# Performance work log

Hardware: AMD Instinct MI355X
Metric: run time of the kernel (lower is better)

The kernel has to match this reference:

```python
import jax, jax.numpy as jnp
import numpy as np

B, T, IN_DIM = 128, 512, 32
H = 256            # h_dim; bidirectional -> embedding_dim D = 2*H = 512
N_EMB = 1024
BETA = 0.25


def setup_inputs() -> dict:
    key = jax.random.key(0)
    ks = jax.random.split(key, 12)
    traj = jax.random.normal(ks[0], (B, T, IN_DIM), dtype=jnp.float32)
    # variable-length padding mask: ones up to length, zeros after
    lengths = jax.random.randint(ks[1], (B,), 1, T + 1)
    mask = (jnp.arange(T)[None, :] < lengths[:, None]).astype(jnp.int32)
    s_x = 1.0 / np.sqrt(H)
    def u(k, shape):
        return jax.random.uniform(k, shape, jnp.float32, -s_x, s_x)
    # PyTorch GRU param layout: W_ih [3H, in], W_hh [3H, H], biases [3H]
    Wx_f, Wh_f = u(ks[2], (3 * H, IN_DIM)), u(ks[3], (3 * H, H))
    bx_f, bh_f = u(ks[4], (3 * H,)), u(ks[5], (3 * H,))
    Wx_b, Wh_b = u(ks[6], (3 * H, IN_DIM)), u(ks[7], (3 * H, H))
    bx_b, bh_b = u(ks[8], (3 * H,)), u(ks[9], (3 * H,))
    # codebook: nn.Embedding(n_embeddings, D) with uniform(-1/n, 1/n) init
    codebook = jax.random.uniform(ks[10], (N_EMB, 2 * H), jnp.float32,
                                  -1.0 / N_EMB, 1.0 / N_EMB)
    return {"traj": traj, "mask": mask,
            "Wx_f": Wx_f, "Wh_f": Wh_f, "bx_f": bx_f, "bh_f": bh_f,
            "Wx_b": Wx_b, "Wh_b": Wh_b, "bx_b": bx_b, "bh_b": bh_b,
            "codebook": codebook}


def _gru_dir(x, Wx, Wh, bx, bh):
    """Single-direction GRU over time (PyTorch gate math). x: [B,T,in] -> [B,T,H]."""
    b, t, _ = x.shape
    h_dim = Wh.shape[1]
    xg = jnp.einsum('bti,gi->btg', x, Wx) + bx  # precompute input gates [B,T,3H]
    def step(h, xg_t):
        hg = h @ Wh.T + bh
        xr, xz, xn = jnp.split(xg_t, 3, axis=-1)
        hr, hz, hn = jnp.split(hg, 3, axis=-1)
        r = jax.nn.sigmoid(xr + hr)
        z = jax.nn.sigmoid(xz + hz)
        n = jnp.tanh(xn + r * hn)
        h_new = (1.0 - z) * n + z * h
        return h_new, h_new
    h0 = jnp.zeros((b, h_dim), x.dtype)
    _, hs = jax.lax.scan(step, h0, jnp.swapaxes(xg, 0, 1))  # [T,B,H]
    return jnp.swapaxes(hs, 0, 1)


def _encode(traj, Wx_f, Wh_f, bx_f, bh_f, Wx_b, Wh_b, bx_b, bh_b):
    out_f = _gru_dir(traj, Wx_f, Wh_f, bx_f, bh_f)
    out_b = jnp.flip(_gru_dir(jnp.flip(traj, axis=1), Wx_b, Wh_b, bx_b, bh_b), axis=1)
    return jnp.concatenate([out_f, out_b], axis=-1)  # [B,T,2H]


def _vq(z_e, codebook, beta):
    # d(z, e) = |z|^2 + |e|^2 - 2 z.e  -> argmin over codebook
    d = (jnp.sum(z_e ** 2, axis=1, keepdims=True)
         + jnp.sum(codebook ** 2, axis=1)[None, :]
         - 2.0 * z_e @ codebook.T)                      # [B, N_EMB]
    idx = jnp.argmin(d, axis=1)                         # [B]
    z_q = codebook[idx]                                 # gather [B, D]
    loss = (jnp.mean((jax.lax.stop_gradient(z_q) - z_e) ** 2)
            + beta * jnp.mean((z_q - jax.lax.stop_gradient(z_e)) ** 2))
    z_q_st = z_e + jax.lax.stop_gradient(z_q - z_e)     # straight-through
    counts = jnp.zeros((codebook.shape[0],), z_e.dtype).at[idx].add(1.0)
    p = counts / z_e.shape[0]
    perplexity = jnp.exp(-jnp.sum(p * jnp.log(p + 1e-10)))
    return loss, z_q_st, perplexity, idx


def reference(traj, mask, Wx_f, Wh_f, bx_f, bh_f, Wx_b, Wh_b, bx_b, bh_b, codebook):
    z_e = _encode(traj, Wx_f, Wh_f, bx_f, bh_f, Wx_b, Wh_b, bx_b, bh_b)  # [B,T,2H]
    t = mask.shape[1]
    # last index where mask == 1:  T-1 - argmax(flip(mask))
    last_real_index = t - 1 - jnp.argmax(jnp.flip(mask, axis=1), axis=1)
    z_e_last = z_e[jnp.arange(z_e.shape[0]), last_real_index]            # [B,2H]
    loss, z_q, perplexity, _ = _vq(z_e_last, codebook, BETA)
    return z_q, loss, perplexity
```

## Files before the change

kernel.cpp:

```cpp
#include <hip/hip_runtime.h>
#include <math.h>

constexpr int B  = 128;
constexpr int T  = 512;
constexpr int IN = 32;
constexpr int H  = 256;
constexpr int D  = 2 * H;
constexpr int NC = 1024;

constexpr int NG   = 64;
constexpr int GW   = 4;
constexpr int SEQ  = 4;
constexpr int NTHR = 768;

constexpr int LDS_PAD_BYTES = 28672;


__global__ void k_zero(int* __restrict__ counts, double* __restrict__ lsum,
                       unsigned long long* __restrict__ slab) {
    const int i = blockIdx.x * 256 + threadIdx.x;
    if (i < NC) counts[i] = 0;
    if (i == 0) *lsum = 0.0;
    slab[i] = 0ull;
}

__global__ void k_lengths(const int* __restrict__ mask, int* __restrict__ last) {
    const int b = blockIdx.x;
    const int t = threadIdx.x;
    int s = 0;
    #pragma unroll
    for (int m = 0; m < T / 64; ++m) s += mask[b * T + m * 64 + t];
    #pragma unroll
    for (int off = 32; off > 0; off >>= 1) s += __shfl_down(s, off, 64);
    if (t == 0) last[b] = s - 1;
}

__global__ void k_plan(const int* __restrict__ last, int* __restrict__ plan,
                       int* __restrict__ slen, int* __restrict__ glen) {
    __shared__ int ll[B];
    const int t = threadIdx.x;
    ll[t] = last[t];
    __syncthreads();
    const int lf = ll[t] + 1;
    const int lb = T - ll[t];
    int rf = 0, rb = 0;
    for (int j = 0; j < B; ++j) {
        const int ljf = ll[j] + 1, ljb = T - ll[j];
        rf += (ljf > lf) || (ljf == lf && j < t);
        rb += (ljb > lb) || (ljb == lb && j < t);
    }
    plan[rf] = t;       slen[rf] = lf;
    plan[128 + rb] = t; slen[128 + rb] = lb;
    if ((rf & 3) == 0) glen[rf >> 2] = lf;
    if ((rb & 3) == 0) glen[32 + (rb >> 2)] = lb;
}

__global__ void k_transpose(float* __restrict__ dst, const float* __restrict__ src,
                            int rows, int cols) {
    const int idx = blockIdx.x * 256 + threadIdx.x;
    const int r = idx % rows;
    const int c = idx / rows;
    dst[idx] = src[r * cols + c];
}

__global__ void k_cbn2(const float* __restrict__ cb, double* __restrict__ cbn2) {
    const int c = blockIdx.x * 256 + threadIdx.x;
    double s = 0.0;
    for (int k = 0; k < D; ++k) {
        const double e = (double)cb[c * D + k];
        s += e * e;
    }
    cbn2[c] = s;
}


__device__ __forceinline__ float sigmoidf_(float x) {
    return 1.0f / (1.0f + expf(-x));
}

__global__ __launch_bounds__(NTHR, 3) void k_gru(
    const float* __restrict__ traj,
    const float* __restrict__ Whf, const float* __restrict__ Whb,
    const float* __restrict__ Wxf, const float* __restrict__ Wxb,
    const float* __restrict__ bxf, const float* __restrict__ bhf,
    const float* __restrict__ bxb, const float* __restrict__ bhb,
    const int* __restrict__ plan, const int* __restrict__ slen,
    const int* __restrict__ glen,
    unsigned long long* __restrict__ hgt,
    float* __restrict__ ze)
{
    extern __shared__ float dynpad[];
    (void)dynpad;

    const int g   = blockIdx.x & 63;
    const int w   = blockIdx.x >> 6;
    const int dir = (g >= 32) ? 1 : 0;

    const float* __restrict__ Wh = dir ? Whb : Whf;
    const float* __restrict__ Wx = dir ? Wxb : Wxf;
    const float* __restrict__ bx = dir ? bxb : bxf;
    const float* __restrict__ bh = dir ? bhb : bhf;

    const int tid = threadIdx.x;
    const int kq  = tid / 96;
    const int rp  = tid - kq * 96;
    const int lr0 = 2 * rp;
    const int gi  = lr0 >> 6;
    const int Rg0 = gi * H + w * 64 + (lr0 & 63);

    __shared__ float4 h4[SEQ][64];
    __shared__ float  P [8][SEQ][194];
    __shared__ float  Px[8][SEQ][194];
    __shared__ float4 xb4[2][SEQ][8];
    __shared__ int    bbS[SEQ], lsS[SEQ];

    if (tid < SEQ) { bbS[tid] = plan[g * 4 + tid]; lsS[tid] = slen[g * 4 + tid]; }
    {
        float2* hp = (float2*)h4;
        if (tid < 512) hp[tid] = make_float2(0.0f, 0.0f);
    }
    const int L = glen[g];

    float4 wh[16];
    {
        const float4* p0 = (const float4*)(Wh + (size_t)Rg0 * 256 + kq * 32);
        const float4* p1 = (const float4*)(Wh + (size_t)(Rg0 + 1) * 256 + kq * 32);
        #pragma unroll
        for (int i = 0; i < 8; ++i) { wh[i] = p0[i]; wh[8 + i] = p1[i]; }
    }
    const float4 wx0 = *(const float4*)(Wx + Rg0 * 32 + kq * 4);
    const float4 wx1 = *(const float4*)(Wx + (Rg0 + 1) * 32 + kq * 4);

    float bxr = 0, bxz = 0, bxn = 0, bhr = 0, bhz = 0, bhn = 0;
    if (tid < 256) {
        const int j2 = tid & 63;
        bxr = bx[w * 64 + j2]; bxz = bx[H + w * 64 + j2]; bxn = bx[2 * H + w * 64 + j2];
        bhr = bh[w * 64 + j2]; bhz = bh[H + w * 64 + j2]; bhn = bh[2 * H + w * 64 + j2];
    }
    __syncthreads();
    if (tid < 128) {
        const int s = tid >> 5, i = tid & 31;
        const int t0 = dir ? (T - 1) : 0;
        ((float*)xb4)[128 + s * 32 + i] = traj[(bbS[s] * T + t0) * IN + i];
    }
    __syncthreads();

    const int u = tid - 256;

    for (int step = 1; step <= L; ++step) {
        const int buf = step & 1;
        unsigned long long* __restrict__ slab =
            hgt + (buf * NG + g) * (GW * SEQ * 64);

        float4 a0 = {0,0,0,0}, a1 = {0,0,0,0}, a2 = {0,0,0,0}, a3 = {0,0,0,0};
        float4 c0 = {0,0,0,0}, c1 = {0,0,0,0}, c2 = {0,0,0,0}, c3 = {0,0,0,0};
        #pragma unroll
        for (int i = 0; i < 8; ++i) {
            const float4 w0 = wh[i];
            const float4 w1 = wh[8 + i];
            float4 hv;
            hv = h4[0][kq * 8 + i];
            a0.x = fmaf(w0.x, hv.x, a0.x); a0.y = fmaf(w0.y, hv.y, a0.y);
            a0.z = fmaf(w0.z, hv.z, a0.z); a0.w = fmaf(w0.w, hv.w, a0.w);
            c0.x = fmaf(w1.x, hv.x, c0.x); c0.y = fmaf(w1.y, hv.y, c0.y);
            c0.z = fmaf(w1.z, hv.z, c0.z); c0.w = fmaf(w1.w, hv.w, c0.w);
            hv = h4[1][kq * 8 + i];
            a1.x = fmaf(w0.x, hv.x, a1.x); a1.y = fmaf(w0.y, hv.y, a1.y);
            a1.z = fmaf(w0.z, hv.z, a1.z); a1.w = fmaf(w0.w, hv.w, a1.w);
            c1.x = fmaf(w1.x, hv.x, c1.x); c1.y = fmaf(w1.y, hv.y, c1.y);
            c1.z = fmaf(w1.z, hv.z, c1.z); c1.w = fmaf(w1.w, hv.w, c1.w);
            hv = h4[2][kq * 8 + i];
            a2.x = fmaf(w0.x, hv.x, a2.x); a2.y = fmaf(w0.y, hv.y, a2.y);
            a2.z = fmaf(w0.z, hv.z, a2.z); a2.w = fmaf(w0.w, hv.w, a2.w);
            c2.x = fmaf(w1.x, hv.x, c2.x); c2.y = fmaf(w1.y, hv.y, c2.y);
            c2.z = fmaf(w1.z, hv.z, c2.z); c2.w = fmaf(w1.w, hv.w, c2.w);
            hv = h4[3][kq * 8 + i];
            a3.x = fmaf(w0.x, hv.x, a3.x); a3.y = fmaf(w0.y, hv.y, a3.y);
            a3.z = fmaf(w0.z, hv.z, a3.z); a3.w = fmaf(w0.w, hv.w, a3.w);
            c3.x = fmaf(w1.x, hv.x, c3.x); c3.y = fmaf(w1.y, hv.y, c3.y);
            c3.z = fmaf(w1.z, hv.z, c3.z); c3.w = fmaf(w1.w, hv.w, c3.w);
        }
        {
            float4 xv;
            float2 pv;
            xv = xb4[buf][0][kq];
            pv.x = a0.x + a0.y + a0.z + a0.w;
            pv.y = c0.x + c0.y + c0.z + c0.w;
            *(float2*)&P[kq][0][lr0] = pv;
            pv.x = wx0.x * xv.x + wx0.y * xv.y + wx0.z * xv.z + wx0.w * xv.w;
            pv.y = wx1.x * xv.x + wx1.y * xv.y + wx1.z * xv.z + wx1.w * xv.w;
            *(float2*)&Px[kq][0][lr0] = pv;
            xv = xb4[buf][1][kq];
            pv.x = a1.x + a1.y + a1.z + a1.w;
            pv.y = c1.x + c1.y + c1.z + c1.w;
            *(float2*)&P[kq][1][lr0] = pv;
            pv.x = wx0.x * xv.x + wx0.y * xv.y + wx0.z * xv.z + wx0.w * xv.w;
            pv.y = wx1.x * xv.x + wx1.y * xv.y + wx1.z * xv.z + wx1.w * xv.w;
            *(float2*)&Px[kq][1][lr0] = pv;
            xv = xb4[buf][2][kq];
            pv.x = a2.x + a2.y + a2.z + a2.w;
            pv.y = c2.x + c2.y + c2.z + c2.w;
            *(float2*)&P[kq][2][lr0] = pv;
            pv.x = wx0.x * xv.x + wx0.y * xv.y + wx0.z * xv.z + wx0.w * xv.w;
            pv.y = wx1.x * xv.x + wx1.y * xv.y + wx1.z * xv.z + wx1.w * xv.w;
            *(float2*)&Px[kq][2][lr0] = pv;
            xv = xb4[buf][3][kq];
            pv.x = a3.x + a3.y + a3.z + a3.w;
            pv.y = c3.x + c3.y + c3.z + c3.w;
            *(float2*)&P[kq][3][lr0] = pv;
            pv.x = wx0.x * xv.x + wx0.y * xv.y + wx0.z * xv.z + wx0.w * xv.w;
            pv.y = wx1.x * xv.x + wx1.y * xv.y + wx1.z * xv.z + wx1.w * xv.w;
            *(float2*)&Px[kq][3][lr0] = pv;
        }
        __syncthreads();

        if (tid < 256) {
            const int j2 = tid & 63, s = tid >> 6;
            float hr = 0.f, hz = 0.f, hn_ = 0.f, xr = 0.f, xz = 0.f, xn = 0.f;
            #pragma unroll
            for (int kk = 0; kk < 8; ++kk) {
                hr  += P [kk][s][j2];
                hz  += P [kk][s][64 + j2];
                hn_ += P [kk][s][128 + j2];
                xr  += Px[kk][s][j2];
                xz  += Px[kk][s][64 + j2];
                xn  += Px[kk][s][128 + j2];
            }
            const float r = sigmoidf_(xr + bxr + hr + bhr);
            const float z = sigmoidf_(xz + bxz + hz + bhz);
            const float n = tanhf(xn + bxn + r * (hn_ + bhn));
            const int jg = w * 64 + j2;
            const float hp = ((const float*)h4)[s * 256 + jg];
            const float hnew = (1.0f - z) * n + z * hp;
            ((float*)h4)[s * 256 + jg] = hnew;
            union { float f; unsigned ui; } cv; cv.f = hnew;
            const unsigned long long pk =
                ((unsigned long long)(unsigned)step << 32) | cv.ui;
            __hip_atomic_store(&slab[w * 256 + s * 64 + j2], pk,
                               __ATOMIC_RELAXED, __HIP_MEMORY_SCOPE_AGENT);
            if (step == lsS[s]) ze[bbS[s] * D + dir * H + jg] = hnew;
        } else {
            float xval = 0.0f;
            int xs = 0, xi = 0;
            const bool do_x = (u < 128) && (step < L);
            if (do_x) {
                xs = u >> 5; xi = u & 31;
                const int tn = dir ? (T - 1 - step) : step;
                xval = traj[(bbS[xs] * T + tn) * IN + xi];
            }
            const int p0 = u >> 8;
            const int r2 = u & 255;
            const int s0 = r2 >> 6, j0 = r2 & 63;
            const int pw0 = p0 + (p0 >= w ? 1 : 0);
            unsigned long long* ad0 = &slab[pw0 * 256 + s0 * 64 + j0];
            if (u < 256) {
                const int pw1 = 2 + (2 >= w ? 1 : 0);
                unsigned long long* ad1 = &slab[pw1 * 256 + s0 * 64 + j0];
                unsigned long long v0 = 0, v1 = 0;
                bool d0 = false, d1 = false;
                do {
                    if (!d0) { v0 = __hip_atomic_load(ad0, __ATOMIC_RELAXED,
                                   __HIP_MEMORY_SCOPE_AGENT); d0 = ((int)(v0 >> 32) >= step); }
                    if (!d1) { v1 = __hip_atomic_load(ad1, __ATOMIC_RELAXED,
                                   __HIP_MEMORY_SCOPE_AGENT); d1 = ((int)(v1 >> 32) >= step); }
                } while (!(d0 && d1));
                union { unsigned ui; float f; } e0, e1;
                e0.ui = (unsigned)v0; e1.ui = (unsigned)v1;
                ((float*)h4)[s0 * 256 + pw0 * 64 + j0] = e0.f;
                ((float*)h4)[s0 * 256 + pw1 * 64 + j0] = e1.f;
            } else {
                unsigned long long v0;
                do {
                    v0 = __hip_atomic_load(ad0, __ATOMIC_RELAXED,
                                           __HIP_MEMORY_SCOPE_AGENT);
                } while ((int)(v0 >> 32) < step);
                union { unsigned ui; float f; } e0; e0.ui = (unsigned)v0;
                ((float*)h4)[s0 * 256 + pw0 * 64 + j0] = e0.f;
            }
            if (do_x)
                ((float*)xb4)[(buf ^ 1) * 128 + xs * 32 + xi] = xval;
        }
        __syncthreads();
    }
}


__global__ __launch_bounds__(256) void k_vq(
    const float* __restrict__ ze, const float* __restrict__ cbT,
    const float* __restrict__ cb, const double* __restrict__ cbn2,
    int* __restrict__ counts, double* __restrict__ lsum,
    float* __restrict__ out)
{
    __shared__ float lz[D];
    __shared__ double ds[256];
    __shared__ int cs[256];

    const int b = blockIdx.x;
    const int t = threadIdx.x;

    lz[t]       = ze[b * D + t];
    lz[t + 256] = ze[b * D + 256 + t];
    __syncthreads();

    double best = 1e300;
    int bc = 0;
    for (int m = 0; m < NC / 256; ++m) {
        const int c = m * 256 + t;
        double s2 = 0.0;
        #pragma unroll 4
        for (int k = 0; k < D; ++k)
            s2 += (double)lz[k] * (double)cbT[k * NC + c];
        const double dist = cbn2[c] - 2.0 * s2;
        if (dist < best) { best = dist; bc = c; }
    }
    ds[t] = best; cs[t] = bc;
    __syncthreads();
    for (int s = 128; s > 0; s >>= 1) {
        if (t < s) {
            if (ds[t + s] < ds[t] || (ds[t + s] == ds[t] && cs[t + s] < cs[t])) {
                ds[t] = ds[t + s]; cs[t] = cs[t + s];
            }
        }
        __syncthreads();
    }
    const int idx = cs[0];
    __syncthreads();

    if (t == 0) atomicAdd(&counts[idx], 1);

    double loc = 0.0;
    for (int jj = t; jj < D; jj += 256) {
        const float zev = lz[jj];
        const float zqv = cb[idx * D + jj];
        out[b * D + jj] = zev + (zqv - zev);
        const double df = (double)zqv - (double)zev;
        loc += df * df;
    }
    ds[t] = loc;
    __syncthreads();
    for (int s = 128; s > 0; s >>= 1) {
        if (t < s) ds[t] += ds[t + s];
        __syncthreads();
    }
    if (t == 0) atomicAdd(lsum, ds[0]);
}

__global__ void k_final(const int* __restrict__ counts,
                        const double* __restrict__ lsum,
                        float* __restrict__ out)
{
    __shared__ double ds[256];
    const int t = threadIdx.x;
    double s = 0.0;
    for (int c = t; c < NC; c += 256) {
        const double p = (double)counts[c] / (double)B;
        s += p * log(p + 1e-10);
    }
    ds[t] = s;
    __syncthreads();
    for (int r = 128; r > 0; r >>= 1) {
        if (t < r) ds[t] += ds[t + r];
        __syncthreads();
    }
    if (t == 0) {
        out[B * D]     = (float)(lsum[0] * 1.25 / (double)(B * D));
        out[B * D + 1] = (float)exp(-ds[0]);
    }
}


extern "C" void kernel_launch(void* const* d_in, const int* in_sizes, int n_in,
                              void* d_out, int out_size, void* d_ws, size_t ws_size,
                              hipStream_t stream) {
    const float* traj = (const float*)d_in[0];
    const int*   mask = (const int*)d_in[1];
    const float* Wxf  = (const float*)d_in[2];
    const float* Whf  = (const float*)d_in[3];
    const float* bxf  = (const float*)d_in[4];
    const float* bhf  = (const float*)d_in[5];
    const float* Wxb  = (const float*)d_in[6];
    const float* Whb  = (const float*)d_in[7];
    const float* bxb  = (const float*)d_in[8];
    const float* bhb  = (const float*)d_in[9];
    const float* cb   = (const float*)d_in[10];
    float* out = (float*)d_out;

    float* ws    = (float*)d_ws;
    float* cbT   = ws;
    float* zebuf = cbT + 524288;
    unsigned long long* hgt =
        (unsigned long long*)(zebuf + 65536);
    int*   last  = (int*)(hgt + 131072);
    int*   plan  = last + 128;
    int*   slen  = plan + 256;
    int*   glen  = slen + 256;
    int*   cnts  = glen + 64;
    double* cbn2 = (double*)(cnts + 1024 + 4);
    double* lsum = cbn2 + 1024;

    k_zero<<<dim3(512), dim3(256), 0, stream>>>(cnts, lsum, hgt);
    k_lengths<<<dim3(B), dim3(64), 0, stream>>>(mask, last);
    k_plan<<<dim3(1), dim3(B), 0, stream>>>(last, plan, slen, glen);

    k_transpose<<<dim3(2048), dim3(256), 0, stream>>>(cbT, cb, NC, D);
    k_cbn2<<<dim3(4), dim3(256), 0, stream>>>(cb, cbn2);

    k_gru<<<dim3(NG * GW), dim3(NTHR), LDS_PAD_BYTES, stream>>>(
        traj, Whf, Whb, Wxf, Wxb, bxf, bhf, bxb, bhb,
        plan, slen, glen, hgt, zebuf);

    k_vq<<<dim3(B), dim3(256), 0, stream>>>(zebuf, cbT, cb, cbn2, cnts, lsum, out);
    k_final<<<dim3(1), dim3(256), 0, stream>>>(cnts, lsum, out);
}
```

Measured before the change: 1.706 ms.

## Claim GRU slots per XCC and poll neighbours through L2-local loads

Each GRU block reads its hardware XCC id and claims a work slot from a per-XCC pool through atomics. It then waits until all four blocks of its group are resident and records whether they share one XCC. When they do, the inter-block hidden-state exchange uses sc0 global loads and stores that stay in the shared L2, instead of agent-scope atomics that go to device-coherent memory. A periodic agent-scope load remains as a fallback. The aim is lower latency for the per-step spin-wait, at the cost of an extra store, a claim handshake, and dependence on XCC placement for correctness.

```diff
diff --git a/kernel.cpp b/kernel.cpp
--- a/kernel.cpp
+++ b/kernel.cpp
@@ -16,11 +16,37 @@
 constexpr int LDS_PAD_BYTES = 28672;
 
 
+__device__ __forceinline__ unsigned long long ld_fast(const unsigned long long* p) {
+    unsigned long long v;
+    asm volatile("global_load_dwordx2 %0, %1, off sc0\n\t"
+                 "s_waitcnt vmcnt(0)"
+                 : "=v"(v) : "v"(p) : "memory");
+    return v;
+}
+
+__device__ __forceinline__ void ld_fast2(const unsigned long long* p0,
+                                         const unsigned long long* p1,
+                                         unsigned long long& v0,
+                                         unsigned long long& v1) {
+    asm volatile("global_load_dwordx2 %0, %2, off sc0\n\t"
+                 "global_load_dwordx2 %1, %3, off sc0\n\t"
+                 "s_waitcnt vmcnt(0)"
+                 : "=&v"(v0), "=&v"(v1) : "v"(p0), "v"(p1) : "memory");
+}
+
+__device__ __forceinline__ void st_fast(unsigned long long* p, unsigned long long v) {
+    asm volatile("global_store_dwordx2 %0, %1, off sc0" :: "v"(p), "v"(v) : "memory");
+}
+
+
 __global__ void k_zero(int* __restrict__ counts, double* __restrict__ lsum,
-                       unsigned long long* __restrict__ slab) {
+                       unsigned long long* __restrict__ slab,
+                       int* __restrict__ claim, int* __restrict__ slotTag) {
     const int i = blockIdx.x * 256 + threadIdx.x;
     if (i < NC) counts[i] = 0;
     if (i == 0) *lsum = 0.0;
+    if (i < 8) claim[i] = 0;
+    if (i < 256) slotTag[i] = 0;
     slab[i] = 0ull;
 }
 
@@ -87,21 +113,56 @@
     const int* __restrict__ plan, const int* __restrict__ slen,
     const int* __restrict__ glen,
     unsigned long long* __restrict__ hgt,
+    int* __restrict__ claim, int* __restrict__ slotTag,
     float* __restrict__ ze)
 {
     extern __shared__ float dynpad[];
     (void)dynpad;
 
-    const int g   = blockIdx.x & 63;
-    const int w   = blockIdx.x >> 6;
-    const int dir = (g >= 32) ? 1 : 0;
+    const int tid = threadIdx.x;
+
+    __shared__ int sSlot, sLoc;
+    if (tid == 0) {
+        int xcc;
+        asm volatile("s_getreg_b32 %0, hwreg(HW_REG_XCC_ID)" : "=s"(xcc));
+        xcc &= 7;
+        int pool = -1, r = 0;
+        for (int t2 = 0; pool < 0; ++t2) {
+            const int x = (xcc + t2) & 7;
+            r = atomicAdd(&claim[x], 1);
+            if (r < 32) pool = x;
+        }
+        const int slot = pool * 32 + r;
+        __hip_atomic_store(&slotTag[slot], 1 + (pool == xcc ? 1 : 0),
+                           __ATOMIC_RELAXED, __HIP_MEMORY_SCOPE_AGENT);
+        const int g0 = slot & ~3;
+        int stat;
+        do {
+            stat = 2;
+            for (int m = 0; m < 4; ++m) {
+                const int tg = __hip_atomic_load(&slotTag[g0 + m],
+                                  __ATOMIC_RELAXED, __HIP_MEMORY_SCOPE_AGENT);
+                if (tg == 0) { stat = 0; break; }
+                if (tg == 1) stat = (stat == 0) ? 0 : 1;
+            }
+            if (stat == 0) __builtin_amdgcn_s_sleep(8);
+        } while (stat == 0);
+        sSlot = slot;
+        sLoc  = (stat == 2);
+    }
+    __syncthreads();
+
+    const int slot = sSlot;
+    const int g    = slot >> 2;
+    const int w    = slot & 3;
+    const bool loc = (sLoc != 0);
+    const int dir  = (g >= 32) ? 1 : 0;
 
     const float* __restrict__ Wh = dir ? Whb : Whf;
     const float* __restrict__ Wx = dir ? Wxb : Wxf;
     const float* __restrict__ bx = dir ? bxb : bxf;
     const float* __restrict__ bh = dir ? bhb : bhf;
 
-    const int tid = threadIdx.x;
     const int kq  = tid / 96;
     const int rp  = tid - kq * 96;
     const int lr0 = 2 * rp;
@@ -236,7 +297,9 @@
             union { float f; unsigned ui; } cv; cv.f = hnew;
             const unsigned long long pk =
                 ((unsigned long long)(unsigned)step << 32) | cv.ui;
-            __hip_atomic_store(&slab[w * 256 + s * 64 + j2], pk,
+            unsigned long long* ad = &slab[w * 256 + s * 64 + j2];
+            if (loc) st_fast(ad, pk);
+            __hip_atomic_store(ad, pk,
                                __ATOMIC_RELAXED, __HIP_MEMORY_SCOPE_AGENT);
             if (step == lsS[s]) ze[bbS[s] * D + dir * H + jg] = hnew;
         } else {
@@ -258,22 +321,59 @@
                 unsigned long long* ad1 = &slab[pw1 * 256 + s0 * 64 + j0];
                 unsigned long long v0 = 0, v1 = 0;
                 bool d0 = false, d1 = false;
-                do {
-                    if (!d0) { v0 = __hip_atomic_load(ad0, __ATOMIC_RELAXED,
-                                   __HIP_MEMORY_SCOPE_AGENT); d0 = ((int)(v0 >> 32) >= step); }
-                    if (!d1) { v1 = __hip_atomic_load(ad1, __ATOMIC_RELAXED,
-                                   __HIP_MEMORY_SCOPE_AGENT); d1 = ((int)(v1 >> 32) >= step); }
-                } while (!(d0 && d1));
+                if (loc) {
+                    int it = 0;
+                    for (;;) {
+                        unsigned long long t0, t1;
+                        ld_fast2(ad0, ad1, t0, t1);
+                        if (!d0 && (int)(t0 >> 32) >= step) { v0 = t0; d0 = true; }
+                        if (!d1 && (int)(t1 >> 32) >= step) { v1 = t1; d1 = true; }
+                        if (d0 && d1) break;
+                        if ((++it & 15) == 0) {
+                            if (!d0) {
+                                t0 = __hip_atomic_load(ad0, __ATOMIC_RELAXED,
+                                                       __HIP_MEMORY_SCOPE_AGENT);
+                                if ((int)(t0 >> 32) >= step) { v0 = t0; d0 = true; }
+                            }
+                            if (!d1) {
+                                t1 = __hip_atomic_load(ad1, __ATOMIC_RELAXED,
+                                                       __HIP_MEMORY_SCOPE_AGENT);
+                                if ((int)(t1 >> 32) >= step) { v1 = t1; d1 = true; }
+                            }
+                            if (d0 && d1) break;
+                        }
+                    }
+                } else {
+                    do {
+                        if (!d0) { v0 = __hip_atomic_load(ad0, __ATOMIC_RELAXED,
+                                       __HIP_MEMORY_SCOPE_AGENT); d0 = ((int)(v0 >> 32) >= step); }
+                        if (!d1) { v1 = __hip_atomic_load(ad1, __ATOMIC_RELAXED,
+                                       __HIP_MEMORY_SCOPE_AGENT); d1 = ((int)(v1 >> 32) >= step); }
+                    } while (!(d0 && d1));
+                }
                 union { unsigned ui; float f; } e0, e1;
                 e0.ui = (unsigned)v0; e1.ui = (unsigned)v1;
                 ((float*)h4)[s0 * 256 + pw0 * 64 + j0] = e0.f;
                 ((float*)h4)[s0 * 256 + pw1 * 64 + j0] = e1.f;
             } else {
                 unsigned long long v0;
-                do {
-                    v0 = __hip_atomic_load(ad0, __ATOMIC_RELAXED,
-                                           __HIP_MEMORY_SCOPE_AGENT);
-                } while ((int)(v0 >> 32) < step);
+                if (loc) {
+                    int it = 0;
+                    for (;;) {
+                        v0 = ld_fast(ad0);
+                        if ((int)(v0 >> 32) >= step) break;
+                        if ((++it & 15) == 0) {
+                            v0 = __hip_atomic_load(ad0, __ATOMIC_RELAXED,
+                                                   __HIP_MEMORY_SCOPE_AGENT);
+                            if ((int)(v0 >> 32) >= step) break;
+                        }
+                    }
+                } else {
+                    do {
+                        v0 = __hip_atomic_load(ad0, __ATOMIC_RELAXED,
+                                               __HIP_MEMORY_SCOPE_AGENT);
+                    } while ((int)(v0 >> 32) < step);
+                }
                 union { unsigned ui; float f; } e0; e0.ui = (unsigned)v0;
                 ((float*)h4)[s0 * 256 + pw0 * 64 + j0] = e0.f;
             }
@@ -397,8 +497,10 @@
     int*   cnts  = glen + 64;
     double* cbn2 = (double*)(cnts + 1024 + 4);
     double* lsum = cbn2 + 1024;
-
-    k_zero<<<dim3(512), dim3(256), 0, stream>>>(cnts, lsum, hgt);
+    int*   claim = (int*)(lsum + 1);
+    int*   slotT = claim + 8;
+
+    k_zero<<<dim3(512), dim3(256), 0, stream>>>(cnts, lsum, hgt, claim, slotT);
     k_lengths<<<dim3(B), dim3(64), 0, stream>>>(mask, last);
     k_plan<<<dim3(1), dim3(B), 0, stream>>>(last, plan, slen, glen);
 
@@ -407,7 +509,7 @@
 
     k_gru<<<dim3(NG * GW), dim3(NTHR), LDS_PAD_BYTES, stream>>>(
         traj, Whf, Whb, Wxf, Wxb, bxf, bhf, bxb, bhb,
-        plan, slen, glen, hgt, zebuf);
+        plan, slen, glen, hgt, claim, slotT, zebuf);
 
     k_vq<<<dim3(B), dim3(256), 0, stream>>>(zebuf, cbT, cb, cbn2, cnts, lsum, out);
     k_final<<<dim3(1), dim3(256), 0, stream>>>(cnts, lsum, out);
```

Measured after the change: 3.265 ms. 91.4% more time.
